# Optimization experiments

Measured on AMD Instinct MI355X. Metric: run time of the kernel, lower is better.

## Reference

```python
import jax, jax.numpy as jnp
import numpy as np

N, E, IN_DIM, HID, HEADS = 50000, 400000, 128, 64, 4
NEG_SLOPE, LN_EPS = 0.2, 1e-5


def setup_inputs() -> dict:
    key = jax.random.key(0)
    ks = jax.random.split(key, 12)
    x = jax.random.normal(ks[0], (N, IN_DIM), dtype=jnp.float32)
    edge_index = jax.random.randint(ks[1], (2, E), 0, N, dtype=jnp.int64)
    s = 1.0 / np.sqrt(HID)
    return {
        "x": x,
        "edge_index": edge_index,
        "W_gcn": jax.random.normal(ks[2], (IN_DIM, HID), dtype=jnp.float32) / np.sqrt(IN_DIM),
        "b_gcn": jnp.zeros((HID,), dtype=jnp.float32),
        "W_gat": jax.random.normal(ks[3], (HID, HEADS * HID), dtype=jnp.float32) * s,
        "att_src": jax.random.normal(ks[4], (HEADS, HID), dtype=jnp.float32) * s,
        "att_dst": jax.random.normal(ks[5], (HEADS, HID), dtype=jnp.float32) * s,
        "b_gat": jnp.zeros((HID,), dtype=jnp.float32),
        "W_patch": jax.random.normal(ks[6], (HID, HID), dtype=jnp.float32) * s,
        "b_patch": jnp.zeros((HID,), dtype=jnp.float32),
        "gamma": jnp.ones((HID,), dtype=jnp.float32),
        "beta": jnp.zeros((HID,), dtype=jnp.float32),
    }


def _forward(x, edge_index, W_gcn, b_gcn, W_gat, att_src, att_dst, b_gat,
             W_patch, b_patch, gamma, beta):
    n = x.shape[0]
    loop = jnp.arange(n, dtype=edge_index.dtype)
    src = jnp.concatenate([edge_index[0], loop])  # self-loops appended (PyG default)
    dst = jnp.concatenate([edge_index[1], loop])

    # ---- GCNConv: symmetric degree normalization + scatter-add ----
    deg = jax.ops.segment_sum(jnp.ones_like(dst, dtype=jnp.float32), dst, num_segments=n)
    dinv = jnp.where(deg > 0, jax.lax.rsqrt(deg), 0.0)
    norm = dinv[src] * dinv[dst]  # [E+N]
    xw = x @ W_gcn  # [N,HID]
    h1 = jax.ops.segment_sum(xw[src] * norm[:, None], dst, num_segments=n) + b_gcn
    h1 = jax.nn.relu(h1)

    # ---- GATConv (heads=4, concat=False -> mean over heads) ----
    z = (h1 @ W_gat).reshape(n, HEADS, HID)  # [N,H,C]
    a_s = jnp.einsum('nhc,hc->nh', z, att_src)  # [N,H]
    a_d = jnp.einsum('nhc,hc->nh', z, att_dst)
    e = jax.nn.leaky_relu(a_s[src] + a_d[dst], negative_slope=NEG_SLOPE)  # [E+N,H]
    # segment-softmax over incoming edges per destination node
    m = jax.ops.segment_max(e, dst, num_segments=n)  # [N,H]
    ex = jnp.exp(e - m[dst])
    denom = jax.ops.segment_sum(ex, dst, num_segments=n)
    alpha = ex / denom[dst]  # [E+N,H]
    agg = jax.ops.segment_sum(z[src] * alpha[:, :, None], dst, num_segments=n)  # [N,H,C]
    h2 = jax.nn.relu(agg.mean(axis=1) + b_gat)

    # ---- residual fusion + LayerNorm (dropout is identity in eval) ----
    h_patch = h1 @ W_patch + b_patch
    h = h1 + h2 + h_patch
    mu = h.mean(axis=-1, keepdims=True)
    var = h.var(axis=-1, keepdims=True)
    return (h - mu) * jax.lax.rsqrt(var + LN_EPS) * gamma + beta


def reference(x, edge_index, W_gcn, b_gcn, W_gat, att_src, att_dst, b_gat,
              W_patch, b_patch, gamma, beta):
    return _forward(x, edge_index, W_gcn, b_gcn, W_gat, att_src, att_dst, b_gat,
                    W_patch, b_patch, gamma, beta)
```

## Files before the change

kernel.cpp:

```cpp
#include <hip/hip_runtime.h>
#include <math.h>

#define IN_DIM 128
#define HID 64
#define HEADS 4
#define NEG_SLOPE 0.2f
#define LN_EPS 1e-5f

typedef short bf16x8 __attribute__((ext_vector_type(8)));
typedef float f32x4  __attribute__((ext_vector_type(4)));

__device__ inline unsigned short f2bf(float f) {
    unsigned u = __float_as_uint(f);
    u += 0x7fffu + ((u >> 16) & 1u);
    return (unsigned short)(u >> 16);
}
__device__ inline float bf2f(unsigned short s) {
    return __uint_as_float(((unsigned)s) << 16);
}
__device__ inline float leaky(float v) { return v > 0.0f ? v : NEG_SLOPE * v; }

__global__ void k_init_all(const unsigned long long* ei, int E, int n,
                           int* flag, int* hist,
                           const float* __restrict__ Wg, const float* __restrict__ Wp,
                           const float* __restrict__ Wgcn,
                           unsigned short* __restrict__ Wt_post,
                           unsigned short* __restrict__ Wt_xw) {
    int nzb = (n + 255) >> 8;
    if ((int)blockIdx.x < nzb) {
        int i = blockIdx.x * 256 + threadIdx.x;
        if (i < n) hist[i] = 0;
        if (blockIdx.x == 0) {
            __shared__ int s_bad;
            if (threadIdx.x == 0) s_bad = 0;
            __syncthreads();
            int lim = E < 4096 ? E : 4096;
            int bad = 0;
            for (int k = threadIdx.x; k < lim; k += 256)
                if (ei[k] >= (unsigned long long)n) bad = 1;
            if (bad) s_bad = 1;
            __syncthreads();
            if (threadIdx.x == 0) *flag = s_bad ? 0 : 1;
        }
    } else {
        int p = (blockIdx.x - nzb) * 256 + threadIdx.x;
        if (p < 2560) {
            int c = p & 63, kg = p >> 6;
            bf16x8 v;
#pragma unroll
            for (int j = 0; j < 8; j++) {
                int k = kg * 8 + j;
                float f;
                if (k < 256) f = 0.25f * Wg[(size_t)(k & 63) * 256 + (k >> 6) * 64 + c];
                else         f = Wp[(size_t)(k - 256) * 64 + c];
                v[j] = (short)f2bf(f);
            }
            *(bf16x8*)(&Wt_post[(size_t)p * 8]) = v;
        } else if (p < 2560 + 1024) {
            int q = p - 2560;
            int c = q & 63, kg = q >> 6;
            bf16x8 v;
#pragma unroll
            for (int j = 0; j < 8; j++)
                v[j] = (short)f2bf(Wgcn[(size_t)(kg * 8 + j) * 64 + c]);
            *(bf16x8*)(&Wt_xw[(size_t)q * 8]) = v;
        }
    }
}

__global__ void k_hist(const void* ei, int E, const int* flag, int* hist) {
    int i = blockIdx.x * blockDim.x + threadIdx.x;
    if (i >= E) return;
    int is64 = *flag;
    int d;
    if (is64) d = (int)((const long long*)ei)[E + i];
    else      d = ((const int*)ei)[E + i];
    atomicAdd(&hist[d], 1);
}

__global__ __launch_bounds__(256) void k_scan1(const int* __restrict__ hist,
                                               int* __restrict__ tmp,
                                               int* __restrict__ partial, int n) {
    __shared__ int s[256];
    int t = threadIdx.x, i = blockIdx.x * 256 + t;
    int v = (i < n) ? hist[i] : 0;
    s[t] = v;
    __syncthreads();
    for (int off = 1; off < 256; off <<= 1) {
        int x = (t >= off) ? s[t - off] : 0;
        __syncthreads();
        s[t] += x;
        __syncthreads();
    }
    tmp[i] = s[t] - v;
    if (t == 255) partial[blockIdx.x] = s[255];
}

__global__ __launch_bounds__(256) void k_scan2_prep(int* partial, int nb,
                                                    const float* __restrict__ Wg,
                                                    const float* __restrict__ att_s,
                                                    const float* __restrict__ att_d,
                                                    float* __restrict__ w_s,
                                                    float* __restrict__ w_d) {
    __shared__ int s[256];
    int t = threadIdx.x;
    int v = (t < nb) ? partial[t] : 0;
    s[t] = v;
    __syncthreads();
    for (int off = 1; off < 256; off <<= 1) {
        int x = (t >= off) ? s[t - off] : 0;
        __syncthreads();
        s[t] += x;
        __syncthreads();
    }
    if (t < nb) partial[t] = s[t] - v;
    int h = t >> 6, k = t & 63;
    float ss = 0.0f, sd = 0.0f;
    for (int c = 0; c < HID; c++) {
        float w = Wg[(size_t)k * (HEADS * HID) + h * HID + c];
        ss += w * att_s[h * HID + c];
        sd += w * att_d[h * HID + c];
    }
    w_s[h * HID + k] = ss;
    w_d[h * HID + k] = sd;
}

__global__ void k_scan3(const int* __restrict__ tmp, const int* __restrict__ partial,
                        const int* __restrict__ hist, int* __restrict__ row_ptr,
                        int* __restrict__ cursor, float* __restrict__ dinv, int n) {
    int i = blockIdx.x * blockDim.x + threadIdx.x;
    if (i >= n) return;
    int v = tmp[i] + partial[i >> 8];
    row_ptr[i] = v;
    cursor[i] = v;
    dinv[i] = rsqrtf((float)(hist[i] + 1));
}

__global__ __launch_bounds__(256) void k_scatter_xw(const void* ei, int E,
                                                    const int* __restrict__ flag,
                                                    int* __restrict__ cursor,
                                                    int* __restrict__ col,
                                                    int* __restrict__ col_d,
                                                    const float* __restrict__ x,
                                                    const unsigned short* __restrict__ Wt_g,
                                                    const float* __restrict__ dinv,
                                                    unsigned short* __restrict__ xws, int n) {
    __shared__ unsigned short Wt[16 * 64 * 8];
    int nsb = (E + 255) >> 8;
    if ((int)blockIdx.x < nsb) {
        int i = blockIdx.x * 256 + threadIdx.x;
        if (i >= E) return;
        int is64 = *flag;
        int s, d;
        if (is64) { s = (int)((const long long*)ei)[i]; d = (int)((const long long*)ei)[E + i]; }
        else      { s = ((const int*)ei)[i];            d = ((const int*)ei)[E + i]; }
        int pos = atomicAdd(&cursor[d], 1);
        col[pos] = s;
        col_d[pos] = d;
    } else {
        int bx = blockIdx.x - nsb;
        int t = threadIdx.x;
        for (int idx = t; idx < 1024; idx += 256)
            *(bf16x8*)(&Wt[idx * 8]) = *(const bf16x8*)(&Wt_g[(size_t)idx * 8]);
        __syncthreads();
        int lane = t & 63;
        int li = lane & 15, quad = lane >> 4;
        int w = t >> 6;
        int r0 = bx * 64 + w * 16;
        int rload = r0 + li; if (rload > n - 1) rload = n - 1;
        f32x4 acc[4];
#pragma unroll
        for (int i = 0; i < 4; i++) acc[i] = (f32x4){0.f, 0.f, 0.f, 0.f};
        const float* xp = x + (size_t)rload * IN_DIM + quad * 8;
#pragma unroll
        for (int ks = 0; ks < 4; ks++) {
            float4 p0 = *(const float4*)(xp + ks * 32);
            float4 p1 = *(const float4*)(xp + ks * 32 + 4);
            bf16x8 a;
            a[0] = (short)f2bf(p0.x); a[1] = (short)f2bf(p0.y);
            a[2] = (short)f2bf(p0.z); a[3] = (short)f2bf(p0.w);
            a[4] = (short)f2bf(p1.x); a[5] = (short)f2bf(p1.y);
            a[6] = (short)f2bf(p1.z); a[7] = (short)f2bf(p1.w);
            int kg = ks * 4 + quad;
#pragma unroll
            for (int tt = 0; tt < 4; tt++) {
                bf16x8 bfr = *(const bf16x8*)(&Wt[((kg * 64) + tt * 16 + li) * 8]);
                acc[tt] = __builtin_amdgcn_mfma_f32_16x16x32_bf16(a, bfr, acc[tt], 0, 0, 0);
            }
        }
#pragma unroll
        for (int reg = 0; reg < 4; reg++) {
            int r = r0 + quad * 4 + reg;
            if (r >= n) continue;
            float dv = dinv[r];
#pragma unroll
            for (int tt = 0; tt < 4; tt++)
                xws[(size_t)r * HID + tt * 16 + li] = f2bf(acc[tt][reg] * dv);
        }
    }
}

__global__ __launch_bounds__(256) void k_gcn(const int* __restrict__ col,
                                             const int* __restrict__ row_ptr,
                                             const int* __restrict__ hist,
                                             const float* __restrict__ dinv,
                                             const unsigned short* __restrict__ xws,
                                             const float* __restrict__ b,
                                             const float* __restrict__ w_s,
                                             const float* __restrict__ w_d,
                                             unsigned short* __restrict__ h1b,
                                             float4* __restrict__ a_s,
                                             float4* __restrict__ a_d, int n) {
    int t = threadIdx.x, c = t & 63;
    int d = blockIdx.x * 4 + (t >> 6);
    if (d >= n) return;
    int start = row_ptr[d], cnt = hist[d];
    float acc = bf2f(xws[(size_t)d * HID + c]);
    int k = 0;
    for (; k + 3 < cnt; k += 4) {
        int s0 = col[start + k],     s1 = col[start + k + 1];
        int s2 = col[start + k + 2], s3 = col[start + k + 3];
        float v0 = bf2f(xws[(size_t)s0 * HID + c]);
        float v1 = bf2f(xws[(size_t)s1 * HID + c]);
        float v2 = bf2f(xws[(size_t)s2 * HID + c]);
        float v3 = bf2f(xws[(size_t)s3 * HID + c]);
        acc += (v0 + v1) + (v2 + v3);
    }
    for (; k < cnt; k++) acc += bf2f(xws[(size_t)col[start + k] * HID + c]);
    float h1c = fmaxf(acc * dinv[d] + b[c], 0.0f);
    h1b[(size_t)d * HID + c] = f2bf(h1c);
    float vs0 = h1c * w_s[c],       vs1 = h1c * w_s[64 + c];
    float vs2 = h1c * w_s[128 + c], vs3 = h1c * w_s[192 + c];
    float vd0 = h1c * w_d[c],       vd1 = h1c * w_d[64 + c];
    float vd2 = h1c * w_d[128 + c], vd3 = h1c * w_d[192 + c];
    for (int o = 32; o > 0; o >>= 1) {
        vs0 += __shfl_xor(vs0, o, 64); vs1 += __shfl_xor(vs1, o, 64);
        vs2 += __shfl_xor(vs2, o, 64); vs3 += __shfl_xor(vs3, o, 64);
        vd0 += __shfl_xor(vd0, o, 64); vd1 += __shfl_xor(vd1, o, 64);
        vd2 += __shfl_xor(vd2, o, 64); vd3 += __shfl_xor(vd3, o, 64);
    }
    if (c == 0) {
        a_s[d] = make_float4(vs0, vs1, vs2, vs3);
        a_d[d] = make_float4(vd0, vd1, vd2, vd3);
    }
}

__global__ void k_ew(const int* __restrict__ col, const int* __restrict__ col_d,
                     const float4* __restrict__ a_s, const float4* __restrict__ a_d,
                     float4* __restrict__ wbuf, int E) {
    int i = blockIdx.x * blockDim.x + threadIdx.x;
    if (i >= E) return;
    int s = col[i], d = col_d[i];
    float4 as = a_s[s], ad = a_d[d];
    float4 r;
    r.x = __expf(leaky(as.x + ad.x));
    r.y = __expf(leaky(as.y + ad.y));
    r.z = __expf(leaky(as.z + ad.z));
    r.w = __expf(leaky(as.w + ad.w));
    wbuf[i] = r;
}

__global__ __launch_bounds__(256) void k_attn(const int* __restrict__ col,
                                              const int* __restrict__ row_ptr,
                                              const int* __restrict__ hist,
                                              const float4* __restrict__ a_s,
                                              const float4* __restrict__ a_d,
                                              const float4* __restrict__ wbuf,
                                              const unsigned short* __restrict__ h1b,
                                              unsigned short* __restrict__ X, int n) {
    int t = threadIdx.x, c = t & 63;
    int d = blockIdx.x * 4 + (t >> 6);
    if (d >= n) return;
    float4 ad = a_d[d];
    float4 asd = a_s[d];
    float w0 = __expf(leaky(asd.x + ad.x));
    float w1 = __expf(leaky(asd.y + ad.y));
    float w2 = __expf(leaky(asd.z + ad.z));
    float w3 = __expf(leaky(asd.w + ad.w));
    float hs = bf2f(h1b[(size_t)d * HID + c]);
    float A0 = w0 * hs, A1 = w1 * hs, A2 = w2 * hs, A3 = w3 * hs;
    float l0 = w0, l1 = w1, l2 = w2, l3 = w3;
    int start = row_ptr[d], cnt = hist[d];
    int k = 0;
    for (; k + 3 < cnt; k += 4) {
        int s0 = col[start + k],     s1 = col[start + k + 1];
        int s2 = col[start + k + 2], s3 = col[start + k + 3];
        float4 e0 = wbuf[start + k],     e1 = wbuf[start + k + 1];
        float4 e2 = wbuf[start + k + 2], e3 = wbuf[start + k + 3];
        float hv0 = bf2f(h1b[(size_t)s0 * HID + c]);
        float hv1 = bf2f(h1b[(size_t)s1 * HID + c]);
        float hv2 = bf2f(h1b[(size_t)s2 * HID + c]);
        float hv3 = bf2f(h1b[(size_t)s3 * HID + c]);
        A0 += e0.x * hv0 + e1.x * hv1 + e2.x * hv2 + e3.x * hv3;
        A1 += e0.y * hv0 + e1.y * hv1 + e2.y * hv2 + e3.y * hv3;
        A2 += e0.z * hv0 + e1.z * hv1 + e2.z * hv2 + e3.z * hv3;
        A3 += e0.w * hv0 + e1.w * hv1 + e2.w * hv2 + e3.w * hv3;
        l0 += (e0.x + e1.x) + (e2.x + e3.x);
        l1 += (e0.y + e1.y) + (e2.y + e3.y);
        l2 += (e0.z + e1.z) + (e2.z + e3.z);
        l3 += (e0.w + e1.w) + (e2.w + e3.w);
    }
    for (; k < cnt; k++) {
        int s0 = col[start + k];
        float4 e0 = wbuf[start + k];
        float hv0 = bf2f(h1b[(size_t)s0 * HID + c]);
        A0 += e0.x * hv0; l0 += e0.x;
        A1 += e0.y * hv0; l1 += e0.y;
        A2 += e0.z * hv0; l2 += e0.z;
        A3 += e0.w * hv0; l3 += e0.w;
    }
    size_t base = (size_t)d * 256;
    X[base + c]       = f2bf(A0 / l0);
    X[base + 64 + c]  = f2bf(A1 / l1);
    X[base + 128 + c] = f2bf(A2 / l2);
    X[base + 192 + c] = f2bf(A3 / l3);
}

__global__ __launch_bounds__(256) void k_post(const unsigned short* __restrict__ Wt_g,
                                              const unsigned short* __restrict__ X,
                                              const unsigned short* __restrict__ h1b,
                                              const float* __restrict__ bp,
                                              const float* __restrict__ bg,
                                              const float* __restrict__ gamma,
                                              const float* __restrict__ beta,
                                              float* __restrict__ out, int n) {
    __shared__ unsigned short Wt[2560 * 8];
    int t = threadIdx.x;
    for (int idx = t; idx < 2560; idx += 256)
        *(bf16x8*)(&Wt[idx * 8]) = *(const bf16x8*)(&Wt_g[(size_t)idx * 8]);
    __syncthreads();

    int lane = t & 63;
    int li = lane & 15, quad = lane >> 4;
    int w = t >> 6;
    int rbase = blockIdx.x * 128 + w * 32;

    f32x4 acc_a[2][4], acc_h[2][4];
#pragma unroll
    for (int rt = 0; rt < 2; rt++)
#pragma unroll
        for (int i = 0; i < 4; i++) {
            acc_a[rt][i] = (f32x4){0.f, 0.f, 0.f, 0.f};
            acc_h[rt][i] = (f32x4){0.f, 0.f, 0.f, 0.f};
        }
#pragma unroll
    for (int ks = 0; ks < 10; ks++) {
        int kg = ks * 4 + quad;
        bf16x8 b0 = *(const bf16x8*)(&Wt[((kg * 64) + 0 * 16 + li) * 8]);
        bf16x8 b1 = *(const bf16x8*)(&Wt[((kg * 64) + 1 * 16 + li) * 8]);
        bf16x8 b2 = *(const bf16x8*)(&Wt[((kg * 64) + 2 * 16 + li) * 8]);
        bf16x8 b3 = *(const bf16x8*)(&Wt[((kg * 64) + 3 * 16 + li) * 8]);
#pragma unroll
        for (int rt = 0; rt < 2; rt++) {
            int row = rbase + rt * 16 + li;
            bf16x8 a;
            if (ks < 8)
                a = *(const bf16x8*)(X + (size_t)row * 256 + quad * 8 + ks * 32);
            else
                a = *(const bf16x8*)(h1b + (size_t)row * HID + quad * 8 + (ks - 8) * 32);
            if (ks < 8) {
                acc_a[rt][0] = __builtin_amdgcn_mfma_f32_16x16x32_bf16(a, b0, acc_a[rt][0], 0, 0, 0);
                acc_a[rt][1] = __builtin_amdgcn_mfma_f32_16x16x32_bf16(a, b1, acc_a[rt][1], 0, 0, 0);
                acc_a[rt][2] = __builtin_amdgcn_mfma_f32_16x16x32_bf16(a, b2, acc_a[rt][2], 0, 0, 0);
                acc_a[rt][3] = __builtin_amdgcn_mfma_f32_16x16x32_bf16(a, b3, acc_a[rt][3], 0, 0, 0);
            } else {
                acc_h[rt][0] = __builtin_amdgcn_mfma_f32_16x16x32_bf16(a, b0, acc_h[rt][0], 0, 0, 0);
                acc_h[rt][1] = __builtin_amdgcn_mfma_f32_16x16x32_bf16(a, b1, acc_h[rt][1], 0, 0, 0);
                acc_h[rt][2] = __builtin_amdgcn_mfma_f32_16x16x32_bf16(a, b2, acc_h[rt][2], 0, 0, 0);
                acc_h[rt][3] = __builtin_amdgcn_mfma_f32_16x16x32_bf16(a, b3, acc_h[rt][3], 0, 0, 0);
            }
        }
    }
    float bgv[4], bpv[4], gv[4], btv[4];
#pragma unroll
    for (int tt = 0; tt < 4; tt++) {
        int c = tt * 16 + li;
        bgv[tt] = bg[c]; bpv[tt] = bp[c]; gv[tt] = gamma[c]; btv[tt] = beta[c];
    }
#pragma unroll
    for (int rt = 0; rt < 2; rt++) {
#pragma unroll
        for (int reg = 0; reg < 4; reg++) {
            int r = rbase + rt * 16 + quad * 4 + reg;
            bool ok = (r < n);
            float hv[4];
            float s1 = 0.0f, s2 = 0.0f;
#pragma unroll
            for (int tt = 0; tt < 4; tt++) {
                int c = tt * 16 + li;
                float h1c = ok ? bf2f(h1b[(size_t)r * HID + c]) : 0.0f;
                float h2 = fmaxf(acc_a[rt][tt][reg] + bgv[tt], 0.0f);
                float h = h1c + h2 + acc_h[rt][tt][reg] + bpv[tt];
                hv[tt] = h;
                s1 += h; s2 += h * h;
            }
            for (int o = 8; o > 0; o >>= 1) {
                s1 += __shfl_xor(s1, o, 64);
                s2 += __shfl_xor(s2, o, 64);
            }
            float mu = s1 * (1.0f / 64.0f);
            float var = s2 * (1.0f / 64.0f) - mu * mu;
            float rs = rsqrtf(var + LN_EPS);
            if (ok) {
#pragma unroll
                for (int tt = 0; tt < 4; tt++) {
                    int c = tt * 16 + li;
                    out[(size_t)r * HID + c] = (hv[tt] - mu) * rs * gv[tt] + btv[tt];
                }
            }
        }
    }
}

extern "C" void kernel_launch(void* const* d_in, const int* in_sizes, int n_in,
                              void* d_out, int out_size, void* d_ws, size_t ws_size,
                              hipStream_t stream) {
    int n = in_sizes[0] / IN_DIM;
    int E = in_sizes[1] / 2;

    const float* x     = (const float*)d_in[0];
    const void*  ei    = d_in[1];
    const float* W_gcn = (const float*)d_in[2];
    const float* b_gcn = (const float*)d_in[3];
    const float* W_gat = (const float*)d_in[4];
    const float* att_s = (const float*)d_in[5];
    const float* att_d = (const float*)d_in[6];
    const float* b_gat = (const float*)d_in[7];
    const float* W_p   = (const float*)d_in[8];
    const float* b_p   = (const float*)d_in[9];
    const float* gamma = (const float*)d_in[10];
    const float* beta  = (const float*)d_in[11];

    int n_pad  = ((n + 255) / 256) * 256;
    int nscan  = n_pad / 256;
    int n128   = ((n + 127) / 128) * 128;
    int nzb    = (n + 255) / 256;
    int nsb    = (E + 255) / 256;

    float* ws = (float*)d_ws;
    size_t off = 0;
    int*   flag    = (int*)(ws + off);  off += 4;
    int*   hist    = (int*)(ws + off);  off += n;
    int*   row_ptr = (int*)(ws + off);  off += n;
    int*   cursor  = (int*)(ws + off);  off += n;
    int*   tmp     = (int*)(ws + off);  off += n_pad;
    int*   partial = (int*)(ws + off);  off += 256;
    int*   colv    = (int*)(ws + off);  off += E;
    int*   col_d   = (int*)(ws + off);  off += E;
    float* dinv    = ws + off;          off += n;
    float* w_s     = ws + off;          off += HEADS * HID;
    float* w_d     = ws + off;          off += HEADS * HID;
    off = (off + 3) & ~(size_t)3;
    unsigned short* Wt_post = (unsigned short*)(ws + off); off += 2560 * 8 / 2;
    unsigned short* Wt_xw   = (unsigned short*)(ws + off); off += 1024 * 8 / 2;
    unsigned short* xws = (unsigned short*)(ws + off); off += (size_t)n * HID / 2;
    off = (off + 3) & ~(size_t)3;
    unsigned short* h1b = (unsigned short*)(ws + off); off += (size_t)n128 * HID / 2;
    off = (off + 3) & ~(size_t)3;
    float4* a_sv   = (float4*)(ws + off); off += (size_t)n * 4;
    float4* a_dv   = (float4*)(ws + off); off += (size_t)n * 4;
    off = (off + 3) & ~(size_t)3;
    float4* wbuf   = (float4*)(ws + off); off += (size_t)E * 4;
    unsigned short* X = (unsigned short*)(ws + off); off += (size_t)n128 * 256 / 2;

    k_init_all<<<nzb + 14, 256, 0, stream>>>((const unsigned long long*)ei, E, n,
                                             flag, hist, W_gat, W_p, W_gcn,
                                             Wt_post, Wt_xw);
    k_hist<<<nsb, 256, 0, stream>>>(ei, E, flag, hist);

    k_scan1<<<nscan, 256, 0, stream>>>(hist, tmp, partial, n);
    k_scan2_prep<<<1, 256, 0, stream>>>(partial, nscan, W_gat, att_s, att_d, w_s, w_d);
    k_scan3<<<nscan, 256, 0, stream>>>(tmp, partial, hist, row_ptr, cursor, dinv, n);

    k_scatter_xw<<<nsb + (n + 63) / 64, 256, 0, stream>>>(ei, E, flag, cursor,
                                                          colv, col_d, x, Wt_xw,
                                                          dinv, xws, n);

    k_gcn<<<(n + 3) / 4, 256, 0, stream>>>(colv, row_ptr, hist, dinv, xws, b_gcn,
                                           w_s, w_d, h1b, a_sv, a_dv, n);

    k_ew<<<(E + 255) / 256, 256, 0, stream>>>(colv, col_d, a_sv, a_dv, wbuf, E);

    k_attn<<<(n + 3) / 4, 256, 0, stream>>>(colv, row_ptr, hist, a_sv, a_dv,
                                            wbuf, h1b, X, n);

    k_post<<<(n + 127) / 128, 256, 0, stream>>>(Wt_post, X, h1b, b_p, b_gat,
                                                gamma, beta, (float*)d_out, n);
}
```

Measured before the change: 240.6 us.

## Fuse edge-weight computation into attention kernel and merge scan passes

```diff
diff --git a/kernel.cpp b/kernel.cpp
--- a/kernel.cpp
+++ b/kernel.cpp
@@ -6,6 +6,7 @@
 #define HEADS 4
 #define NEG_SLOPE 0.2f
 #define LN_EPS 1e-5f
+#define ECAP 512
 
 typedef short bf16x8 __attribute__((ext_vector_type(8)));
 typedef float f32x4  __attribute__((ext_vector_type(4)));
@@ -24,26 +25,32 @@
                            int* flag, int* hist,
                            const float* __restrict__ Wg, const float* __restrict__ Wp,
                            const float* __restrict__ Wgcn,
+                           const float* __restrict__ att_s, const float* __restrict__ att_d,
                            unsigned short* __restrict__ Wt_post,
-                           unsigned short* __restrict__ Wt_xw) {
+                           unsigned short* __restrict__ Wt_xw,
+                           float* __restrict__ w_s, float* __restrict__ w_d) {
     int nzb = (n + 255) >> 8;
+    int t = threadIdx.x;
     if ((int)blockIdx.x < nzb) {
-        int i = blockIdx.x * 256 + threadIdx.x;
+        int i = blockIdx.x * 256 + t;
         if (i < n) hist[i] = 0;
         if (blockIdx.x == 0) {
             __shared__ int s_bad;
-            if (threadIdx.x == 0) s_bad = 0;
+            if (t == 0) s_bad = 0;
             __syncthreads();
             int lim = E < 4096 ? E : 4096;
             int bad = 0;
-            for (int k = threadIdx.x; k < lim; k += 256)
+            for (int k = t; k < lim; k += 256)
                 if (ei[k] >= (unsigned long long)n) bad = 1;
             if (bad) s_bad = 1;
             __syncthreads();
-            if (threadIdx.x == 0) *flag = s_bad ? 0 : 1;
-        }
-    } else {
-        int p = (blockIdx.x - nzb) * 256 + threadIdx.x;
+            if (t == 0) *flag = s_bad ? 0 : 1;
+        }
+        return;
+    }
+    int role = blockIdx.x - nzb;
+    if (role < 14) {
+        int p = role * 256 + t;
         if (p < 2560) {
             int c = p & 63, kg = p >> 6;
             bf16x8 v;
@@ -65,6 +72,16 @@
                 v[j] = (short)f2bf(Wgcn[(size_t)(kg * 8 + j) * 64 + c]);
             *(bf16x8*)(&Wt_xw[(size_t)q * 8]) = v;
         }
+    } else {
+        int h = t >> 6, k = t & 63;
+        float ss = 0.0f, sd = 0.0f;
+        for (int c = 0; c < HID; c++) {
+            float w = Wg[(size_t)k * (HEADS * HID) + h * HID + c];
+            ss += w * att_s[h * HID + c];
+            sd += w * att_d[h * HID + c];
+        }
+        w_s[h * HID + k] = ss;
+        w_d[h * HID + k] = sd;
     }
 }
 
@@ -96,15 +113,17 @@
     if (t == 255) partial[blockIdx.x] = s[255];
 }
 
-__global__ __launch_bounds__(256) void k_scan2_prep(int* partial, int nb,
-                                                    const float* __restrict__ Wg,
-                                                    const float* __restrict__ att_s,
-                                                    const float* __restrict__ att_d,
-                                                    float* __restrict__ w_s,
-                                                    float* __restrict__ w_d) {
+__global__ __launch_bounds__(256) void k_scan_apply(const int* __restrict__ tmp,
+                                                    const int* __restrict__ partial,
+                                                    const int* __restrict__ hist,
+                                                    int* __restrict__ row_ptr,
+                                                    int* __restrict__ cursor,
+                                                    float* __restrict__ dinv,
+                                                    int n, int nscan) {
     __shared__ int s[256];
+    __shared__ int excl_s;
     int t = threadIdx.x;
-    int v = (t < nb) ? partial[t] : 0;
+    int v = (t < nscan) ? partial[t] : 0;
     s[t] = v;
     __syncthreads();
     for (int off = 1; off < 256; off <<= 1) {
@@ -113,34 +132,22 @@
         s[t] += x;
         __syncthreads();
     }
-    if (t < nb) partial[t] = s[t] - v;
-    int h = t >> 6, k = t & 63;
-    float ss = 0.0f, sd = 0.0f;
-    for (int c = 0; c < HID; c++) {
-        float w = Wg[(size_t)k * (HEADS * HID) + h * HID + c];
-        ss += w * att_s[h * HID + c];
-        sd += w * att_d[h * HID + c];
-    }
-    w_s[h * HID + k] = ss;
-    w_d[h * HID + k] = sd;
-}
-
-__global__ void k_scan3(const int* __restrict__ tmp, const int* __restrict__ partial,
-                        const int* __restrict__ hist, int* __restrict__ row_ptr,
-                        int* __restrict__ cursor, float* __restrict__ dinv, int n) {
-    int i = blockIdx.x * blockDim.x + threadIdx.x;
-    if (i >= n) return;
-    int v = tmp[i] + partial[i >> 8];
-    row_ptr[i] = v;
-    cursor[i] = v;
-    dinv[i] = rsqrtf((float)(hist[i] + 1));
+    if (t == 0) excl_s = (blockIdx.x == 0) ? 0 : s[blockIdx.x - 1];
+    __syncthreads();
+    int excl = excl_s;
+    int i = blockIdx.x * 256 + t;
+    if (i < n) {
+        int v2 = tmp[i] + excl;
+        row_ptr[i] = v2;
+        cursor[i] = v2;
+        dinv[i] = rsqrtf((float)(hist[i] + 1));
+    }
 }
 
 __global__ __launch_bounds__(256) void k_scatter_xw(const void* ei, int E,
                                                     const int* __restrict__ flag,
                                                     int* __restrict__ cursor,
                                                     int* __restrict__ col,
-                                                    int* __restrict__ col_d,
                                                     const float* __restrict__ x,
                                                     const unsigned short* __restrict__ Wt_g,
                                                     const float* __restrict__ dinv,
@@ -156,7 +163,6 @@
         else      { s = ((const int*)ei)[i];            d = ((const int*)ei)[E + i]; }
         int pos = atomicAdd(&cursor[d], 1);
         col[pos] = s;
-        col_d[pos] = d;
     } else {
         int bx = blockIdx.x - nsb;
         int t = threadIdx.x;
@@ -245,33 +251,53 @@
     }
 }
 
-__global__ void k_ew(const int* __restrict__ col, const int* __restrict__ col_d,
-                     const float4* __restrict__ a_s, const float4* __restrict__ a_d,
-                     float4* __restrict__ wbuf, int E) {
-    int i = blockIdx.x * blockDim.x + threadIdx.x;
-    if (i >= E) return;
-    int s = col[i], d = col_d[i];
-    float4 as = a_s[s], ad = a_d[d];
-    float4 r;
-    r.x = __expf(leaky(as.x + ad.x));
-    r.y = __expf(leaky(as.y + ad.y));
-    r.z = __expf(leaky(as.z + ad.z));
-    r.w = __expf(leaky(as.w + ad.w));
-    wbuf[i] = r;
-}
-
 __global__ __launch_bounds__(256) void k_attn(const int* __restrict__ col,
                                               const int* __restrict__ row_ptr,
                                               const int* __restrict__ hist,
                                               const float4* __restrict__ a_s,
                                               const float4* __restrict__ a_d,
-                                              const float4* __restrict__ wbuf,
                                               const unsigned short* __restrict__ h1b,
                                               unsigned short* __restrict__ X, int n) {
-    int t = threadIdx.x, c = t & 63;
-    int d = blockIdx.x * 4 + (t >> 6);
+    __shared__ float4 wls[ECAP];
+    __shared__ int    sls[ECAP];
+    __shared__ int    sb[5];
+    __shared__ float4 sad[4];
+    int t = threadIdx.x;
+    int d0 = blockIdx.x * 4;
+    if (t == 0) {
+        int bptr = row_ptr[d0];
+        sb[0] = bptr;
+        for (int j = 0; j < 4; j++) {
+            int d = d0 + j;
+            bptr += (d < n) ? hist[d] : 0;
+            sb[j + 1] = bptr;
+        }
+    }
+    if (t < 4 && d0 + t < n) sad[t] = a_d[d0 + t];
+    __syncthreads();
+    int start0 = sb[0];
+    int totc = sb[4] - start0;
+    int rel1 = sb[1] - start0, rel2 = sb[2] - start0, rel3 = sb[3] - start0;
+    bool fast = (totc <= ECAP);
+    if (fast) {
+        for (int e = t; e < totc; e += 256) {
+            int s = col[start0 + e];
+            int j = (e >= rel1) + (e >= rel2) + (e >= rel3);
+            float4 as = a_s[s], ad = sad[j];
+            float4 w;
+            w.x = __expf(leaky(as.x + ad.x));
+            w.y = __expf(leaky(as.y + ad.y));
+            w.z = __expf(leaky(as.z + ad.z));
+            w.w = __expf(leaky(as.w + ad.w));
+            wls[e] = w;
+            sls[e] = s;
+        }
+    }
+    __syncthreads();
+    int c = t & 63, w = t >> 6;
+    int d = d0 + w;
     if (d >= n) return;
-    float4 ad = a_d[d];
+    float4 ad = sad[w];
     float4 asd = a_s[d];
     float w0 = __expf(leaky(asd.x + ad.x));
     float w1 = __expf(leaky(asd.y + ad.y));
@@ -280,34 +306,48 @@
     float hs = bf2f(h1b[(size_t)d * HID + c]);
     float A0 = w0 * hs, A1 = w1 * hs, A2 = w2 * hs, A3 = w3 * hs;
     float l0 = w0, l1 = w1, l2 = w2, l3 = w3;
-    int start = row_ptr[d], cnt = hist[d];
-    int k = 0;
-    for (; k + 3 < cnt; k += 4) {
-        int s0 = col[start + k],     s1 = col[start + k + 1];
-        int s2 = col[start + k + 2], s3 = col[start + k + 3];
-        float4 e0 = wbuf[start + k],     e1 = wbuf[start + k + 1];
-        float4 e2 = wbuf[start + k + 2], e3 = wbuf[start + k + 3];
-        float hv0 = bf2f(h1b[(size_t)s0 * HID + c]);
-        float hv1 = bf2f(h1b[(size_t)s1 * HID + c]);
-        float hv2 = bf2f(h1b[(size_t)s2 * HID + c]);
-        float hv3 = bf2f(h1b[(size_t)s3 * HID + c]);
-        A0 += e0.x * hv0 + e1.x * hv1 + e2.x * hv2 + e3.x * hv3;
-        A1 += e0.y * hv0 + e1.y * hv1 + e2.y * hv2 + e3.y * hv3;
-        A2 += e0.z * hv0 + e1.z * hv1 + e2.z * hv2 + e3.z * hv3;
-        A3 += e0.w * hv0 + e1.w * hv1 + e2.w * hv2 + e3.w * hv3;
-        l0 += (e0.x + e1.x) + (e2.x + e3.x);
-        l1 += (e0.y + e1.y) + (e2.y + e3.y);
-        l2 += (e0.z + e1.z) + (e2.z + e3.z);
-        l3 += (e0.w + e1.w) + (e2.w + e3.w);
-    }
-    for (; k < cnt; k++) {
-        int s0 = col[start + k];
-        float4 e0 = wbuf[start + k];
-        float hv0 = bf2f(h1b[(size_t)s0 * HID + c]);
-        A0 += e0.x * hv0; l0 += e0.x;
-        A1 += e0.y * hv0; l1 += e0.y;
-        A2 += e0.z * hv0; l2 += e0.z;
-        A3 += e0.w * hv0; l3 += e0.w;
+    int lo = sb[w] - start0, hi = sb[w + 1] - start0;
+    if (fast) {
+        int k = lo;
+        for (; k + 3 < hi; k += 4) {
+            int s0 = sls[k], s1 = sls[k + 1], s2 = sls[k + 2], s3 = sls[k + 3];
+            float4 e0 = wls[k], e1 = wls[k + 1], e2 = wls[k + 2], e3 = wls[k + 3];
+            float hv0 = bf2f(h1b[(size_t)s0 * HID + c]);
+            float hv1 = bf2f(h1b[(size_t)s1 * HID + c]);
+            float hv2 = bf2f(h1b[(size_t)s2 * HID + c]);
+            float hv3 = bf2f(h1b[(size_t)s3 * HID + c]);
+            A0 += e0.x * hv0 + e1.x * hv1 + e2.x * hv2 + e3.x * hv3;
+            A1 += e0.y * hv0 + e1.y * hv1 + e2.y * hv2 + e3.y * hv3;
+            A2 += e0.z * hv0 + e1.z * hv1 + e2.z * hv2 + e3.z * hv3;
+            A3 += e0.w * hv0 + e1.w * hv1 + e2.w * hv2 + e3.w * hv3;
+            l0 += (e0.x + e1.x) + (e2.x + e3.x);
+            l1 += (e0.y + e1.y) + (e2.y + e3.y);
+            l2 += (e0.z + e1.z) + (e2.z + e3.z);
+            l3 += (e0.w + e1.w) + (e2.w + e3.w);
+        }
+        for (; k < hi; k++) {
+            int s0 = sls[k];
+            float4 e0 = wls[k];
+            float hv0 = bf2f(h1b[(size_t)s0 * HID + c]);
+            A0 += e0.x * hv0; l0 += e0.x;
+            A1 += e0.y * hv0; l1 += e0.y;
+            A2 += e0.z * hv0; l2 += e0.z;
+            A3 += e0.w * hv0; l3 += e0.w;
+        }
+    } else {
+        for (int k = lo; k < hi; k++) {
+            int s0 = col[start0 + k];
+            float4 as = a_s[s0];
+            float u0 = __expf(leaky(as.x + ad.x));
+            float u1 = __expf(leaky(as.y + ad.y));
+            float u2 = __expf(leaky(as.z + ad.z));
+            float u3 = __expf(leaky(as.w + ad.w));
+            float hv0 = bf2f(h1b[(size_t)s0 * HID + c]);
+            A0 += u0 * hv0; l0 += u0;
+            A1 += u1 * hv0; l1 += u1;
+            A2 += u2 * hv0; l2 += u2;
+            A3 += u3 * hv0; l3 += u3;
+        }
     }
     size_t base = (size_t)d * 256;
     X[base + c]       = f2bf(A0 / l0);
@@ -446,7 +486,6 @@
     int*   tmp     = (int*)(ws + off);  off += n_pad;
     int*   partial = (int*)(ws + off);  off += 256;
     int*   colv    = (int*)(ws + off);  off += E;
-    int*   col_d   = (int*)(ws + off);  off += E;
     float* dinv    = ws + off;          off += n;
     float* w_s     = ws + off;          off += HEADS * HID;
     float* w_d     = ws + off;          off += HEADS * HID;
@@ -460,29 +499,26 @@
     float4* a_sv   = (float4*)(ws + off); off += (size_t)n * 4;
     float4* a_dv   = (float4*)(ws + off); off += (size_t)n * 4;
     off = (off + 3) & ~(size_t)3;
-    float4* wbuf   = (float4*)(ws + off); off += (size_t)E * 4;
     unsigned short* X = (unsigned short*)(ws + off); off += (size_t)n128 * 256 / 2;
 
-    k_init_all<<<nzb + 14, 256, 0, stream>>>((const unsigned long long*)ei, E, n,
+    k_init_all<<<nzb + 15, 256, 0, stream>>>((const unsigned long long*)ei, E, n,
                                              flag, hist, W_gat, W_p, W_gcn,
-                                             Wt_post, Wt_xw);
+                                             att_s, att_d, Wt_post, Wt_xw, w_s, w_d);
     k_hist<<<nsb, 256, 0, stream>>>(ei, E, flag, hist);
 
     k_scan1<<<nscan, 256, 0, stream>>>(hist, tmp, partial, n);
-    k_scan2_prep<<<1, 256, 0, stream>>>(partial, nscan, W_gat, att_s, att_d, w_s, w_d);
-    k_scan3<<<nscan, 256, 0, stream>>>(tmp, partial, hist, row_ptr, cursor, dinv, n);
+    k_scan_apply<<<nscan, 256, 0, stream>>>(tmp, partial, hist, row_ptr, cursor,
+                                            dinv, n, nscan);
 
     k_scatter_xw<<<nsb + (n + 63) / 64, 256, 0, stream>>>(ei, E, flag, cursor,
-                                                          colv, col_d, x, Wt_xw,
+                                                          colv, x, Wt_xw,
                                                           dinv, xws, n);
 
     k_gcn<<<(n + 3) / 4, 256, 0, stream>>>(colv, row_ptr, hist, dinv, xws, b_gcn,
                                            w_s, w_d, h1b, a_sv, a_dv, n);
 
-    k_ew<<<(E + 255) / 256, 256, 0, stream>>>(colv, col_d, a_sv, a_dv, wbuf, E);
-
     k_attn<<<(n + 3) / 4, 256, 0, stream>>>(colv, row_ptr, hist, a_sv, a_dv,
-                                            wbuf, h1b, X, n);
+                                            h1b, X, n);
 
     k_post<<<(n + 127) / 128, 256, 0, stream>>>(Wt_post, X, h1b, b_p, b_gat,
                                                 gamma, beta, (float*)d_out, n);
```

After: 226.0 us. -6.1%, faster.
